# Kernel tuning notes

Hardware: AMD Instinct MI355X
Metric: run time of the kernel (lower is better)

The kernel has to match this reference:

```python
import jax, jax.numpy as jnp
import numpy as np

EMBED_DIM = 1024
NUM_HEADS = 16
HEAD_DIM = EMBED_DIM // NUM_HEADS


def setup_inputs() -> dict:
    key = jax.random.key(0)
    ks = jax.random.split(key, 9)
    B, S, E = 2, 2048, EMBED_DIM
    scale = 1.0 / np.sqrt(E)
    x = jax.random.normal(ks[0], (B, S, E), dtype=jnp.float32)
    Wq = jax.random.normal(ks[1], (E, E), dtype=jnp.float32) * scale
    bq = jax.random.normal(ks[2], (E,), dtype=jnp.float32) * 0.01
    Wk = jax.random.normal(ks[3], (E, E), dtype=jnp.float32) * scale
    bk = jax.random.normal(ks[4], (E,), dtype=jnp.float32) * 0.01
    Wv = jax.random.normal(ks[5], (E, E), dtype=jnp.float32) * scale
    bv = jax.random.normal(ks[6], (E,), dtype=jnp.float32) * 0.01
    Wo = jax.random.normal(ks[7], (E, E), dtype=jnp.float32) * scale
    bo = jax.random.normal(ks[8], (E,), dtype=jnp.float32) * 0.01
    return {"x": x, "Wq": Wq, "bq": bq, "Wk": Wk, "bk": bk,
            "Wv": Wv, "bv": bv, "Wo": Wo, "bo": bo}


def reference(x, Wq, bq, Wk, bk, Wv, bv, Wo, bo):
    B, S, E = x.shape
    H, D = NUM_HEADS, HEAD_DIM
    # projections (torch Linear: x @ W.T + b), reshape to (B, H, S, D)
    q = (x @ Wq.T + bq).reshape(B, S, H, D).transpose(0, 2, 1, 3)
    k = (x @ Wk.T + bk).reshape(B, S, H, D).transpose(0, 2, 1, 3)
    v = (x @ Wv.T + bv).reshape(B, S, H, D).transpose(0, 2, 1, 3)
    softmax_scale = 1.0 / np.sqrt(D)
    # (B, H, S, S) scores, causal mask, stable softmax
    scores = softmax_scale * jnp.einsum('bhsd,bhtd->bhst', q, k)
    causal = jnp.tril(jnp.ones((S, S), dtype=bool))  # True = keep
    scores = jnp.where(causal, scores, -jnp.inf)
    attn = jax.nn.softmax(scores, axis=-1)
    out = jnp.einsum('bhst,bhtd->bhsd', attn, v)  # (B, H, S, D)
    out = out.transpose(0, 2, 1, 3).reshape(B, S, E)
    return out @ Wo.T + bo
```

## Files before the change

### kernel.cpp

```cpp
#include <hip/hip_runtime.h>
#include <cstdint>
#include <cstddef>

#define SEQ   2048
#define BATCH 2
#define EMB   1024
#define NH    16
#define HD    64
#define MTOT  (BATCH * SEQ)
#define NX    (MTOT * EMB)
#define NW    (EMB * EMB)

typedef __bf16 bf16_t;
typedef __bf16 bf16x4 __attribute__((ext_vector_type(4)));
typedef __bf16 bf16x8 __attribute__((ext_vector_type(8)));
typedef float  f32x4  __attribute__((ext_vector_type(4)));
typedef float  f32x16 __attribute__((ext_vector_type(16)));

__device__ __forceinline__ f32x4 mfma16(bf16x8 a, bf16x8 b, f32x4 c) {
  return __builtin_amdgcn_mfma_f32_16x16x32_bf16(a, b, c, 0, 0, 0);
}
__device__ __forceinline__ f32x16 mfma32(bf16x8 a, bf16x8 b, f32x16 c) {
  return __builtin_amdgcn_mfma_f32_32x32x16_bf16(a, b, c, 0, 0, 0);
}

__global__ __launch_bounds__(256) void cvt_all(
    const float* __restrict__ x,  const float* __restrict__ wq,
    const float* __restrict__ wk, const float* __restrict__ wv,
    const float* __restrict__ wo,
    bf16_t* __restrict__ xb,  bf16_t* __restrict__ wqb,
    bf16_t* __restrict__ wkb, bf16_t* __restrict__ wvb,
    bf16_t* __restrict__ wob) {
  long e = ((long)blockIdx.x * 256 + threadIdx.x) * 4;
  const float* s; bf16_t* d; long off;
  if (e < NX) { s = x; d = xb; off = e; }
  else {
    long e2 = e - NX;
    int w = (int)(e2 >> 20);
    off = e2 & (NW - 1);
    s = (w == 0) ? wq : (w == 1) ? wk : (w == 2) ? wv : wo;
    d = (w == 0) ? wqb : (w == 1) ? wkb : (w == 2) ? wvb : wob;
  }
  float4 v = *(const float4*)(s + off);
  bf16x4 o;
  o[0] = (bf16_t)v.x; o[1] = (bf16_t)v.y; o[2] = (bf16_t)v.z; o[3] = (bf16_t)v.w;
  *(bf16x4*)(d + off) = o;
}

template <typename OT>
__global__ __launch_bounds__(256) void gemm_bt3(
    const bf16_t* __restrict__ A,
    const bf16_t* __restrict__ W0, const bf16_t* __restrict__ W1,
    const bf16_t* __restrict__ W2,
    const float* __restrict__ b0, const float* __restrict__ b1,
    const float* __restrict__ b2,
    OT* __restrict__ C0, OT* __restrict__ C1, OT* __restrict__ C2) {
  constexpr int K = EMB, N = EMB, BK = 32;
  const int z = blockIdx.z;
  const bf16_t* B    = (z == 0) ? W0 : (z == 1) ? W1 : W2;
  const float*  bias = (z == 0) ? b0 : (z == 1) ? b1 : b2;
  OT*           C    = (z == 0) ? C0 : (z == 1) ? C1 : C2;

  __shared__ __align__(16) bf16_t As[2][128 * BK];
  __shared__ __align__(16) bf16_t Bs[2][128 * BK];

  const int tid  = threadIdx.x;
  const int lane = tid & 63;
  const int wave = tid >> 6;
  const int quad = lane >> 4;
  const int l16  = lane & 15;
  const int wm   = (wave >> 1) * 64;
  const int wn   = (wave & 1) * 64;
  const int m0   = blockIdx.y * 128;
  const int n0   = blockIdx.x * 128;

  const int c0 = tid, c1 = tid + 256;
  const bf16_t* ga0 = A + (size_t)(m0 + (c0 >> 2)) * K + (c0 & 3) * 8;
  const bf16_t* ga1 = A + (size_t)(m0 + (c1 >> 2)) * K + (c1 & 3) * 8;
  const bf16_t* gb0 = B + (size_t)(n0 + (c0 >> 2)) * K + (c0 & 3) * 8;
  const bf16_t* gb1 = B + (size_t)(n0 + (c1 >> 2)) * K + (c1 & 3) * 8;
  const int lo0 = c0 * 8, lo1 = c1 * 8;

  uint4 ra0 = *(const uint4*)ga0;
  uint4 ra1 = *(const uint4*)ga1;
  uint4 rb0 = *(const uint4*)gb0;
  uint4 rb1 = *(const uint4*)gb1;

  f32x4 acc[4][4] = {};

  for (int kk = 0; kk < K; kk += BK) {
    const int cur = (kk >> 5) & 1;
    *(uint4*)&As[cur][lo0] = ra0;
    *(uint4*)&As[cur][lo1] = ra1;
    *(uint4*)&Bs[cur][lo0] = rb0;
    *(uint4*)&Bs[cur][lo1] = rb1;
    __syncthreads();

    if (kk + BK < K) {
      ra0 = *(const uint4*)(ga0 + kk + BK);
      ra1 = *(const uint4*)(ga1 + kk + BK);
      rb0 = *(const uint4*)(gb0 + kk + BK);
      rb1 = *(const uint4*)(gb1 + kk + BK);
    }

    bf16x8 af[4], bfr[4];
#pragma unroll
    for (int i = 0; i < 4; ++i)
      af[i] = *(const bf16x8*)&As[cur][(wm + i * 16 + l16) * BK + quad * 8];
#pragma unroll
    for (int j = 0; j < 4; ++j)
      bfr[j] = *(const bf16x8*)&Bs[cur][(wn + j * 16 + l16) * BK + quad * 8];
#pragma unroll
    for (int i = 0; i < 4; ++i)
#pragma unroll
      for (int j = 0; j < 4; ++j)
        acc[i][j] = mfma16(af[i], bfr[j], acc[i][j]);
  }

#pragma unroll
  for (int j = 0; j < 4; ++j) {
    const int col = n0 + wn + j * 16 + l16;
    const float bv = bias[col];
#pragma unroll
    for (int i = 0; i < 4; ++i) {
      const int row = m0 + wm + i * 16 + quad * 4;
#pragma unroll
      for (int r = 0; r < 4; ++r) {
        C[(size_t)(row + r) * N + col] = (OT)(acc[i][j][r] + bv);
      }
    }
  }
}

__global__ __launch_bounds__(256) void attn128(
    const bf16_t* __restrict__ Qg, const bf16_t* __restrict__ Kg,
    const bf16_t* __restrict__ Vg, bf16_t* __restrict__ Og) {
  const int hb  = blockIdx.x;
  const int y   = blockIdx.y;
  const int s   = (y < 8) ? (15 - y) : (y - 8);
  const int h   = hb & 15, b = hb >> 4;
  const int tid = threadIdx.x;
  const int lane = tid & 63, wave = tid >> 6;
  const int l31 = lane & 31, hi = lane >> 5;

  __shared__ __align__(16) bf16_t Ks[2][64 * 72];
  __shared__ __align__(16) bf16_t VsT[2][64 * 72];
  __shared__ __align__(16) bf16_t PQ[128 * 72];

  const size_t base = ((size_t)b * SEQ) * EMB + (size_t)h * HD;
  const bf16_t* Kp = Kg + base;
  const bf16_t* Vp = Vg + base;

  const int kr0r = tid >> 3, kcol = (tid & 7) * 8;
  const int kr1r = kr0r + 32;
  const int vt = tid & 63, vd0 = (tid >> 6) * 8;

  bf16_t* Pw = &PQ[wave * (32 * 72)];

  const int q0  = s * 128;
  const int nit = 2 * s + 2;
  const bf16_t* Qp = Qg + base + (size_t)q0 * EMB;

  uint4 kr0  = *(const uint4*)(Kp + (size_t)kr0r * EMB + kcol);
  uint4 kr1  = *(const uint4*)(Kp + (size_t)kr1r * EMB + kcol);
  bf16x8 vr0 = *(const bf16x8*)(Vp + (size_t)vt * EMB + vd0);
  bf16x8 vr1 = *(const bf16x8*)(Vp + (size_t)vt * EMB + vd0 + 32);

#pragma unroll
  for (int i = 0; i < 4; ++i) {
    const int c = tid + 256 * i;
    *(uint4*)&PQ[(c >> 3) * 72 + (c & 7) * 8] =
        *(const uint4*)(Qp + (size_t)(c >> 3) * EMB + (c & 7) * 8);
  }
  __syncthreads();

  bf16x8 qf[4];
#pragma unroll
  for (int kk = 0; kk < 4; ++kk)
    qf[kk] = *(const bf16x8*)&PQ[(32 * wave + l31) * 72 + kk * 16 + hi * 8];

  f32x16 acc_o0 = {}, acc_o1 = {};
  float l_i[16];
#pragma unroll
  for (int r = 0; r < 16; ++r) l_i[r] = 0.f;

  for (int it = 0; it < nit; ++it) {
    bf16_t* Kc = &Ks[it & 1][0];
    bf16_t* Vc = &VsT[it & 1][0];
    *(uint4*)&Kc[kr0r * 72 + kcol] = kr0;
    *(uint4*)&Kc[kr1r * 72 + kcol] = kr1;
#pragma unroll
    for (int u = 0; u < 8; ++u) {
      Vc[(vd0 + u) * 72 + vt]      = vr0[u];
      Vc[(vd0 + 32 + u) * 72 + vt] = vr1[u];
    }
    __syncthreads();

    if (it + 1 < nit) {
      const bf16_t* Kn = Kp + (size_t)(it + 1) * 64 * EMB;
      const bf16_t* Vn = Vp + (size_t)(it + 1) * 64 * EMB;
      kr0 = *(const uint4*)(Kn + (size_t)kr0r * EMB + kcol);
      kr1 = *(const uint4*)(Kn + (size_t)kr1r * EMB + kcol);
      vr0 = *(const bf16x8*)(Vn + (size_t)vt * EMB + vd0);
      vr1 = *(const bf16x8*)(Vn + (size_t)vt * EMB + vd0 + 32);
    }

    const bool active = (64 * it <= q0 + 32 * wave + 31);
    if (active) {
      f32x16 acc0 = {}, acc1 = {};
#pragma unroll
      for (int kk = 0; kk < 4; ++kk) {
        const bf16x8 kf0 = *(const bf16x8*)&Kc[l31 * 72 + kk * 16 + hi * 8];
        const bf16x8 kf1 =
            *(const bf16x8*)&Kc[(32 + l31) * 72 + kk * 16 + hi * 8];
        acc0 = mfma32(qf[kk], kf0, acc0);
        acc1 = mfma32(qf[kk], kf1, acc1);
      }

      constexpr float SC2 = 0.18033688011112042f;
      if (it >= nit - 2) {
        const int row0 = q0 + 32 * wave + 4 * hi;
        const int c0 = 64 * it + l31, c1 = c0 + 32;
#pragma unroll
        for (int r = 0; r < 16; ++r) {
          const int row = row0 + (r & 3) + 8 * (r >> 2);
          float p0 = exp2f(__builtin_fmaf(acc0[r], SC2, -8.f));
          float p1 = exp2f(__builtin_fmaf(acc1[r], SC2, -8.f));
          if (c0 > row) p0 = 0.f;
          if (c1 > row) p1 = 0.f;
          l_i[r] += p0 + p1;
          const int rl = (r & 3) + 8 * (r >> 2) + 4 * hi;
          Pw[rl * 72 + l31]      = (bf16_t)p0;
          Pw[rl * 72 + 32 + l31] = (bf16_t)p1;
        }
      } else {
#pragma unroll
        for (int r = 0; r < 16; ++r) {
          const float p0 = exp2f(__builtin_fmaf(acc0[r], SC2, -8.f));
          const float p1 = exp2f(__builtin_fmaf(acc1[r], SC2, -8.f));
          l_i[r] += p0 + p1;
          const int rl = (r & 3) + 8 * (r >> 2) + 4 * hi;
          Pw[rl * 72 + l31]      = (bf16_t)p0;
          Pw[rl * 72 + 32 + l31] = (bf16_t)p1;
        }
      }

#pragma unroll
      for (int kk = 0; kk < 4; ++kk) {
        const bf16x8 pf = *(const bf16x8*)&Pw[l31 * 72 + kk * 16 + hi * 8];
        const bf16x8 vf0 = *(const bf16x8*)&Vc[l31 * 72 + kk * 16 + hi * 8];
        const bf16x8 vf1 =
            *(const bf16x8*)&Vc[(32 + l31) * 72 + kk * 16 + hi * 8];
        acc_o0 = mfma32(pf, vf0, acc_o0);
        acc_o1 = mfma32(pf, vf1, acc_o1);
      }
    }
  }

  bf16_t* Op = Og + base + (size_t)(q0 + 32 * wave) * EMB;
#pragma unroll
  for (int r = 0; r < 16; ++r) {
    float rs = l_i[r];
#pragma unroll
    for (int off = 1; off < 32; off <<= 1) rs += __shfl_xor(rs, off, 64);
    const float inv = 1.f / rs;
    const int rl = (r & 3) + 8 * (r >> 2) + 4 * hi;
    Op[(size_t)rl * EMB + l31]      = (bf16_t)(acc_o0[r] * inv);
    Op[(size_t)rl * EMB + 32 + l31] = (bf16_t)(acc_o1[r] * inv);
  }
}

extern "C" void kernel_launch(void* const* d_in, const int* in_sizes, int n_in,
                              void* d_out, int out_size, void* d_ws,
                              size_t ws_size, hipStream_t stream) {
  const float* x  = (const float*)d_in[0];
  const float* Wq = (const float*)d_in[1];
  const float* bq = (const float*)d_in[2];
  const float* Wk = (const float*)d_in[3];
  const float* bk = (const float*)d_in[4];
  const float* Wv = (const float*)d_in[5];
  const float* bv = (const float*)d_in[6];
  const float* Wo = (const float*)d_in[7];
  const float* bo = (const float*)d_in[8];
  float* out = (float*)d_out;

  char* p = (char*)d_ws;
  bf16_t* xb  = (bf16_t*)p; p += (size_t)NX * 2;
  bf16_t* wqb = (bf16_t*)p; p += (size_t)NW * 2;
  bf16_t* wkb = (bf16_t*)p; p += (size_t)NW * 2;
  bf16_t* wvb = (bf16_t*)p; p += (size_t)NW * 2;
  bf16_t* wob = (bf16_t*)p; p += (size_t)NW * 2;
  bf16_t* qb  = (bf16_t*)p; p += (size_t)NX * 2;
  bf16_t* kb  = (bf16_t*)p; p += (size_t)NX * 2;
  bf16_t* vb  = (bf16_t*)p; p += (size_t)NX * 2;
  bf16_t* ab  = (bf16_t*)p; p += (size_t)NX * 2;

  const int ntot = NX + 4 * NW;
  cvt_all<<<dim3(ntot / 4 / 256), 256, 0, stream>>>(
      x, Wq, Wk, Wv, Wo, xb, wqb, wkb, wvb, wob);

  gemm_bt3<bf16_t><<<dim3(EMB / 128, MTOT / 128, 3), 256, 0, stream>>>(
      xb, wqb, wkb, wvb, bq, bk, bv, qb, kb, vb);

  attn128<<<dim3(BATCH * NH, SEQ / 128), 256, 0, stream>>>(qb, kb, vb, ab);

  gemm_bt3<float><<<dim3(EMB / 128, MTOT / 128, 1), 256, 0, stream>>>(
      ab, wob, wob, wob, bo, bo, bo, out, out, out);
}
```

Before: 215.2 us.

## Load GEMM MFMA fragments directly from global memory, dropping LDS staging

Measured after the change: 300.9 us. +39.8%, slower.

```diff
diff --git a/kernel.cpp b/kernel.cpp
--- a/kernel.cpp
+++ b/kernel.cpp
@@ -55,14 +55,11 @@
     const float* __restrict__ b0, const float* __restrict__ b1,
     const float* __restrict__ b2,
     OT* __restrict__ C0, OT* __restrict__ C1, OT* __restrict__ C2) {
-  constexpr int K = EMB, N = EMB, BK = 32;
+  constexpr int K = EMB, N = EMB;
   const int z = blockIdx.z;
   const bf16_t* B    = (z == 0) ? W0 : (z == 1) ? W1 : W2;
   const float*  bias = (z == 0) ? b0 : (z == 1) ? b1 : b2;
   OT*           C    = (z == 0) ? C0 : (z == 1) ? C1 : C2;
-
-  __shared__ __align__(16) bf16_t As[2][128 * BK];
-  __shared__ __align__(16) bf16_t Bs[2][128 * BK];
 
   const int tid  = threadIdx.x;
   const int lane = tid & 63;
@@ -74,42 +71,24 @@
   const int m0   = blockIdx.y * 128;
   const int n0   = blockIdx.x * 128;
 
-  const int c0 = tid, c1 = tid + 256;
-  const bf16_t* ga0 = A + (size_t)(m0 + (c0 >> 2)) * K + (c0 & 3) * 8;
-  const bf16_t* ga1 = A + (size_t)(m0 + (c1 >> 2)) * K + (c1 & 3) * 8;
-  const bf16_t* gb0 = B + (size_t)(n0 + (c0 >> 2)) * K + (c0 & 3) * 8;
-  const bf16_t* gb1 = B + (size_t)(n0 + (c1 >> 2)) * K + (c1 & 3) * 8;
-  const int lo0 = c0 * 8, lo1 = c1 * 8;
-
-  uint4 ra0 = *(const uint4*)ga0;
-  uint4 ra1 = *(const uint4*)ga1;
-  uint4 rb0 = *(const uint4*)gb0;
-  uint4 rb1 = *(const uint4*)gb1;
+  const bf16_t* ap[4];
+  const bf16_t* bp[4];
+#pragma unroll
+  for (int i = 0; i < 4; ++i)
+    ap[i] = A + (size_t)(m0 + wm + i * 16 + l16) * K + quad * 8;
+#pragma unroll
+  for (int j = 0; j < 4; ++j)
+    bp[j] = B + (size_t)(n0 + wn + j * 16 + l16) * K + quad * 8;
 
   f32x4 acc[4][4] = {};
 
-  for (int kk = 0; kk < K; kk += BK) {
-    const int cur = (kk >> 5) & 1;
-    *(uint4*)&As[cur][lo0] = ra0;
-    *(uint4*)&As[cur][lo1] = ra1;
-    *(uint4*)&Bs[cur][lo0] = rb0;
-    *(uint4*)&Bs[cur][lo1] = rb1;
-    __syncthreads();
-
-    if (kk + BK < K) {
-      ra0 = *(const uint4*)(ga0 + kk + BK);
-      ra1 = *(const uint4*)(ga1 + kk + BK);
-      rb0 = *(const uint4*)(gb0 + kk + BK);
-      rb1 = *(const uint4*)(gb1 + kk + BK);
-    }
-
+#pragma unroll 4
+  for (int kk = 0; kk < K; kk += 32) {
     bf16x8 af[4], bfr[4];
 #pragma unroll
-    for (int i = 0; i < 4; ++i)
-      af[i] = *(const bf16x8*)&As[cur][(wm + i * 16 + l16) * BK + quad * 8];
-#pragma unroll
-    for (int j = 0; j < 4; ++j)
-      bfr[j] = *(const bf16x8*)&Bs[cur][(wn + j * 16 + l16) * BK + quad * 8];
+    for (int i = 0; i < 4; ++i) af[i]  = *(const bf16x8*)(ap[i] + kk);
+#pragma unroll
+    for (int j = 0; j < 4; ++j) bfr[j] = *(const bf16x8*)(bp[j] + kk);
 #pragma unroll
     for (int i = 0; i < 4; ++i)
 #pragma unroll
```
